# Kernel tuning notes

Hardware: AMD Instinct MI355X
Metric: run time of the kernel (lower is better)

## Reference

```python
import jax, jax.numpy as jnp
import numpy as np

EPS = 1e-8
N_NODES, N_EDGES = 10000, 160000
SI, VI = 128, 16          # node scalar / vector channels
ES, EV = 32, 4            # edge scalar / vector channels
SO, VO = 128, 16          # output scalar / vector channels
MSI, MVI = 2 * SI + ES, 2 * VI + EV   # message input dims: 288, 36
H1 = max(MVI, VO)         # layer-1 hidden = 36 (bottleneck=1)
H2 = max(VO, VO)          # layer-2 hidden = 16
SVO = 3                   # scalarization_vectorization_output_dim


def _safe_norm(x, axis):
    return jnp.sqrt(jnp.sum(x * x, axis=axis) + EPS)


def _gcp(s, v, frames, Wdown, Wdf, Wso, bso, Wup, Wg, bg):
    """GCP block on edge-level inputs (node_inputs=False, vector_gate=True).
    s: [E, si], v: [E, vi, 3], frames: [E, 3, 3]."""
    v_pre = jnp.swapaxes(v, -1, -2)                 # [E, 3, vi]
    v_hid = v_pre @ Wdown                           # [E, 3, h]
    v_norm = _safe_norm(v_hid, axis=-2)             # [E, h]
    v_frames = v_pre @ Wdf                          # [E, 3, svo]
    # scalarize: frames @ v_frames -> [E,3,svo], transpose -> [E,svo,3], flatten to 9
    local = jnp.swapaxes(frames @ v_frames, -1, -2).reshape(v.shape[0], 3 * SVO)
    merged = jnp.concatenate([s, v_norm, local], axis=-1)
    s_out = merged @ Wso + bso                      # [E, so]
    v_out = jnp.swapaxes(v_hid @ Wup, -1, -2)       # [E, vo, 3]
    gate = jax.nn.sigmoid(jax.nn.silu(s_out) @ Wg + bg)  # vector gate
    v_out = v_out * gate[..., None]
    return jax.nn.silu(s_out), v_out


def _lin(key, fan_in, fan_out):
    return jax.random.normal(key, (fan_in, fan_out), dtype=jnp.float32) / np.sqrt(fan_in)


def setup_inputs() -> dict:
    key = jax.random.key(0)
    ks = jax.random.split(key, 24)
    M1 = H1 + MSI + 3 * SVO   # 333
    M2 = H2 + SO + 3 * SVO    # 153
    return {
        "node_s": jax.random.normal(ks[0], (N_NODES, SI), dtype=jnp.float32),
        "node_v": jax.random.normal(ks[1], (N_NODES, VI, 3), dtype=jnp.float32),
        "edge_s": jax.random.normal(ks[2], (N_EDGES, ES), dtype=jnp.float32),
        "edge_v": jax.random.normal(ks[3], (N_EDGES, EV, 3), dtype=jnp.float32),
        "frames": jax.random.normal(ks[4], (N_EDGES, 3, 3), dtype=jnp.float32),
        "g1_Wdown": _lin(ks[5], MVI, H1),
        "g1_Wdf": _lin(ks[6], MVI, SVO),
        "g1_Wso": _lin(ks[7], M1, SO),
        "g1_bso": jnp.zeros((SO,), dtype=jnp.float32),
        "g1_Wup": _lin(ks[8], H1, VO),
        "g1_Wg": _lin(ks[9], SO, VO),
        "g1_bg": jnp.zeros((VO,), dtype=jnp.float32),
        "g2_Wdown": _lin(ks[10], VO, H2),
        "g2_Wdf": _lin(ks[11], VO, SVO),
        "g2_Wso": _lin(ks[12], M2, SO),
        "g2_bso": jnp.zeros((SO,), dtype=jnp.float32),
        "g2_Wup": _lin(ks[13], H2, VO),
        "g2_Wg": _lin(ks[14], SO, VO),
        "g2_bg": jnp.zeros((VO,), dtype=jnp.float32),
        "att_W": _lin(ks[15], SO, 1),
        "att_b": jnp.zeros((1,), dtype=jnp.float32),
        "edge_index": jax.random.randint(ks[16], (2, N_EDGES), 0, N_NODES, dtype=jnp.int64),
    }


def reference(node_s, node_v, edge_s, edge_v, frames,
              g1_Wdown, g1_Wdf, g1_Wso, g1_bso, g1_Wup, g1_Wg, g1_bg,
              g2_Wdown, g2_Wdf, g2_Wso, g2_bso, g2_Wup, g2_Wg, g2_bg,
              att_W, att_b, edge_index):
    row, col = edge_index[0], edge_index[1]
    # edge gather: concat source node, edge, dest node features
    ms = jnp.concatenate([node_s[row], edge_s, node_s[col]], axis=-1)   # [E, 288]
    mv = jnp.concatenate([node_v[row], edge_v, node_v[col]], axis=1)    # [E, 36, 3]
    # message_fusion[0]
    s, v = _gcp(ms, mv, frames, g1_Wdown, g1_Wdf, g1_Wso, g1_bso, g1_Wup, g1_Wg, g1_bg)
    # message_fusion[1] with residual
    s2, v2 = _gcp(s, v, frames, g2_Wdown, g2_Wdf, g2_Wso, g2_bso, g2_Wup, g2_Wg, g2_bg)
    s, v = s + s2, v + v2
    # scalar message attention
    attn = jax.nn.sigmoid(s @ att_W + att_b)
    s = s * attn
    # flatten ScalarVector and scatter-sum aggregate to destination nodes
    flat = jnp.concatenate([s, v.reshape(v.shape[0], VO * 3)], axis=-1)  # [E, 176]
    agg = jax.ops.segment_sum(flat, row, num_segments=N_NODES)           # [N, 176]
    return agg
```

## Files before the change

kernel.cpp:

```cpp
#include <hip/hip_runtime.h>
#include <hip/hip_bf16.h>

#define E_TOT 160000
#define NN    10000
#define EPB   32

typedef unsigned short ushortT;
typedef unsigned int   uintT;
typedef __attribute__((ext_vector_type(8))) short short8;
typedef __attribute__((ext_vector_type(4))) float f32x4;

__device__ __forceinline__ float sigmoidf_(float x) { return 1.0f / (1.0f + __expf(-x)); }
__device__ __forceinline__ float siluf_(float x) { return x * sigmoidf_(x); }

__device__ __forceinline__ ushortT f2b(float f) {
    union { float f; uintT u; } x; x.f = f;
    uintT r = x.u + 0x7fffu + ((x.u >> 16) & 1u);
    return (ushortT)(r >> 16);
}
__device__ __forceinline__ float b2f(ushortT h) {
    union { uintT u; float f; } x; x.u = ((uintT)h) << 16; return x.f;
}
__device__ __forceinline__ uintT pk2(float lo, float hi) {
    union { __hip_bfloat162 h; uintT u; } cv;
    cv.h = __float22bfloat162_rn(make_float2(lo, hi));
    return cv.u;
}
__device__ __forceinline__ short8 ldfrag(const float* p) {
    const float4 x = ((const float4*)p)[0];
    const float4 y = ((const float4*)p)[1];
    union { uintT u[4]; short8 s; } r;
    r.u[0] = pk2(x.x, x.y); r.u[1] = pk2(x.z, x.w);
    r.u[2] = pk2(y.x, y.y); r.u[3] = pk2(y.z, y.w);
    return r.s;
}

#define OFF_W1SO 0
#define OFF_W2SO 45056
#define OFF_W1DF 65536
#define OFF_W1G  68608
#define OFF_W1UP 70656
#define OFF_W2DF 71680
#define OFF_W2G  72704
#define OFF_W2UP 74752
#define WT_USH   75264

#define NOFF_OFF   56320000ULL
#define CUR_OFF    56360016ULL
#define WT_OFF     57040032ULL
#define WS_CSR     57190560ULL
#define NS16_OFF   57190560ULL
#define WS_NS      59750560ULL
#define ES16_OFF   59750560ULL
#define WS_ES      69990560ULL

__device__ __forceinline__ bool idx_is64(const int* pi) {
    return (pi[1] | pi[3] | pi[5] | pi[7] | pi[9] | pi[11] | pi[13] | pi[15]) == 0;
}

__device__ __forceinline__ void weight_prep(
    int i,
    const float* __restrict__ W1so, const float* __restrict__ W2so,
    const float* __restrict__ W1d,  const float* __restrict__ W1f,
    const float* __restrict__ W1g,  const float* __restrict__ W1up,
    const float* __restrict__ W2d,  const float* __restrict__ W2f,
    const float* __restrict__ W2g,  const float* __restrict__ W2up,
    ushortT* __restrict__ ws)
{
    if (i < OFF_W2SO) {
        int n = i / 352, k = i - n * 352;
        ws[i] = (k < 333) ? f2b(W1so[k * 128 + n]) : (ushortT)0;
    } else if (i < OFF_W1DF) {
        int j = i - OFF_W2SO, n = j / 160, k = j - n * 160;
        ws[i] = (k < 153) ? f2b(W2so[k * 128 + n]) : (ushortT)0;
    } else if (i < OFF_W1G) {
        int j = i - OFF_W1DF, n = j / 64, k = j - n * 64;
        float v = 0.f;
        if (k < 36) { if (n < 36) v = W1d[k * 36 + n]; else if (n < 39) v = W1f[k * 3 + (n - 36)]; }
        ws[i] = f2b(v);
    } else if (i < OFF_W1UP) {
        int j = i - OFF_W1G, n = j / 128, k = j - n * 128;
        ws[i] = f2b(W1g[k * 16 + n]);
    } else if (i < OFF_W2DF) {
        int j = i - OFF_W1UP, n = j / 64, k = j - n * 64;
        ws[i] = (k < 36) ? f2b(W1up[k * 16 + n]) : (ushortT)0;
    } else if (i < OFF_W2G) {
        int j = i - OFF_W2DF, n = j / 32, k = j - n * 32;
        float v = 0.f;
        if (k < 16) { if (n < 16) v = W2d[k * 16 + n]; else if (n < 19) v = W2f[k * 3 + (n - 16)]; }
        ws[i] = f2b(v);
    } else if (i < OFF_W2UP) {
        int j = i - OFF_W2G, n = j / 128, k = j - n * 128;
        ws[i] = f2b(W2g[k * 16 + n]);
    } else if (i < WT_USH) {
        int j = i - OFF_W2UP, n = j / 32, k = j - n * 32;
        ws[i] = (k < 16) ? f2b(W2up[k * 16 + n]) : (ushortT)0;
    }
}

__global__ __launch_bounds__(256) void setup_kernel(
    const float* __restrict__ W1so, const float* __restrict__ W2so,
    const float* __restrict__ W1d,  const float* __restrict__ W1f,
    const float* __restrict__ W1g,  const float* __restrict__ W1up,
    const float* __restrict__ W2d,  const float* __restrict__ W2f,
    const float* __restrict__ W2g,  const float* __restrict__ W2up,
    ushortT* __restrict__ ws,
    const void* __restrict__ eidx, int* __restrict__ cur,
    const float* __restrict__ node_s, const float* __restrict__ edge_s,
    ushortT* __restrict__ ns16, ushortT* __restrict__ es16)
{
    int i = blockIdx.x * 256 + threadIdx.x;
    {
        const int* pi = (const int*)eidx;
        const long long* pl = (const long long*)eidx;
        int r = idx_is64(pi) ? (int)pl[i] : pi[i];
        atomicAdd(&cur[r], 1);
    }
    if (ns16 && i < 160000) {
        float4 x = ((const float4*)node_s)[i * 2];
        float4 y = ((const float4*)node_s)[i * 2 + 1];
        uint4 st;
        st.x = pk2(x.x, x.y); st.y = pk2(x.z, x.w);
        st.z = pk2(y.x, y.y); st.w = pk2(y.z, y.w);
        ((uint4*)ns16)[i] = st;
    }
    if (es16) {
        #pragma unroll
        for (int k = 0; k < 4; ++k) {
            float4 x = ((const float4*)edge_s)[i * 8 + 2 * k];
            float4 y = ((const float4*)edge_s)[i * 8 + 2 * k + 1];
            uint4 st;
            st.x = pk2(x.x, x.y); st.y = pk2(x.z, x.w);
            st.z = pk2(y.x, y.y); st.w = pk2(y.z, y.w);
            ((uint4*)es16)[i * 4 + k] = st;
        }
    }
    weight_prep(i, W1so, W2so, W1d, W1f, W1g, W1up, W2d, W2f, W2g, W2up, ws);
}

__global__ __launch_bounds__(256) void prep_kernel(
    const float* __restrict__ W1so, const float* __restrict__ W2so,
    const float* __restrict__ W1d,  const float* __restrict__ W1f,
    const float* __restrict__ W1g,  const float* __restrict__ W1up,
    const float* __restrict__ W2d,  const float* __restrict__ W2f,
    const float* __restrict__ W2g,  const float* __restrict__ W2up,
    ushortT* __restrict__ ws, float* __restrict__ out)
{
    int i = blockIdx.x * 256 + threadIdx.x;
    float4* o4 = (float4*)out;
    #pragma unroll
    for (int k = 0; k < 6; ++k) {
        int z = i + k * 75264;
        if (z < 440000) o4[z] = make_float4(0.f, 0.f, 0.f, 0.f);
    }
    weight_prep(i, W1so, W2so, W1d, W1f, W1g, W1up, W2d, W2f, W2g, W2up, ws);
}

__global__ __launch_bounds__(256) void scan_kernel(int* __restrict__ cur,
                                                   int* __restrict__ noff)
{
    __shared__ int buf[10000];
    __shared__ int partial[256];
    const int t = threadIdx.x;
    for (int i = t; i < NN; i += 256) buf[i] = cur[i];
    for (int i = t; i < NN; i += 256) cur[i] = 0;
    __syncthreads();
    const int base = t * 40;
    int s = 0;
    #pragma unroll
    for (int i = 0; i < 40; ++i) s += (base + i < NN) ? buf[base + i] : 0;
    partial[t] = s;
    __syncthreads();
    for (int o = 1; o < 256; o <<= 1) {
        int v = (t >= o) ? partial[t - o] : 0;
        __syncthreads();
        partial[t] += v;
        __syncthreads();
    }
    int run = (t == 0) ? 0 : partial[t - 1];
    #pragma unroll
    for (int i = 0; i < 40; ++i) {
        int gi = base + i;
        if (gi < NN) { int v = buf[gi]; noff[gi] = run; run += v; }
    }
    if (t == 255) noff[NN] = partial[255];
}

__global__ __launch_bounds__(256) void node_kernel(const ushortT* __restrict__ fb,
                                                   const int* __restrict__ noff,
                                                   float* __restrict__ out)
{
    const int w = threadIdx.x >> 6, l = threadIdx.x & 63;
    const int n = blockIdx.x * 4 + w;
    if (l >= 44) return;
    const int s = noff[n], eend = noff[n + 1];
    float a0 = 0.f, a1 = 0.f, a2 = 0.f, a3 = 0.f;
    int idx = s;
    for (; idx + 2 <= eend; idx += 2) {
        uint2 p0 = *(const uint2*)(fb + (size_t)idx * 176 + l * 4);
        uint2 p1 = *(const uint2*)(fb + (size_t)(idx + 1) * 176 + l * 4);
        a0 += b2f((ushortT)(p0.x & 0xffff)); a1 += b2f((ushortT)(p0.x >> 16));
        a2 += b2f((ushortT)(p0.y & 0xffff)); a3 += b2f((ushortT)(p0.y >> 16));
        a0 += b2f((ushortT)(p1.x & 0xffff)); a1 += b2f((ushortT)(p1.x >> 16));
        a2 += b2f((ushortT)(p1.y & 0xffff)); a3 += b2f((ushortT)(p1.y >> 16));
    }
    if (idx < eend) {
        uint2 p0 = *(const uint2*)(fb + (size_t)idx * 176 + l * 4);
        a0 += b2f((ushortT)(p0.x & 0xffff)); a1 += b2f((ushortT)(p0.x >> 16));
        a2 += b2f((ushortT)(p0.y & 0xffff)); a3 += b2f((ushortT)(p0.y >> 16));
    }
    ((float4*)(out + (size_t)n * 176))[l] = make_float4(a0, a1, a2, a3);
}

#define MFMA(a, b, c) __builtin_amdgcn_mfma_f32_16x16x32_bf16((a), (b), (c), 0, 0, 0)

__global__ __launch_bounds__(256, 5) void edge_kernel(
    const float* __restrict__ node_s, const float* __restrict__ node_v,
    const float* __restrict__ edge_s, const float* __restrict__ edge_v,
    const float* __restrict__ frames,
    const float* __restrict__ b1so, const float* __restrict__ b1g,
    const float* __restrict__ b2so, const float* __restrict__ b2g,
    const float* __restrict__ attW, const float* __restrict__ attb,
    const ushortT* __restrict__ wsc,
    const void* __restrict__ eidx, float* __restrict__ out,
    ushortT* __restrict__ fb, int* __restrict__ cur, const int* __restrict__ noff,
    const ushortT* __restrict__ ns16, const ushortT* __restrict__ es16,
    int csr)
{
    const ushortT* W1T   = wsc + OFF_W1SO;
    const ushortT* W2T   = wsc + OFF_W2SO;
    const ushortT* W1dfT = wsc + OFF_W1DF;
    const ushortT* W1gT  = wsc + OFF_W1G;
    const ushortT* W1upT = wsc + OFF_W1UP;
    const ushortT* W2dfT = wsc + OFF_W2DF;
    const ushortT* W2gT  = wsc + OFF_W2G;
    const ushortT* W2upT = wsc + OFF_W2UP;

    __shared__ __align__(16) char smem[31232];
    ushortT* mvA     = (ushortT*)smem;
    ushortT* m2      = (ushortT*)smem;
    ushortT* vhidA   = (ushortT*)(smem + 10752);
    ushortT* s2s     = (ushortT*)(smem + 10752);
    ushortT* normbuf = (ushortT*)(smem + 19456);
    ushortT* v1A     = (ushortT*)(smem + 19456);
    ushortT* vhid2A  = (ushortT*)(smem + 24064);
    float*   vfr2f   = (float*)(smem + 28672);
    float*   fr      = (float*)(smem + 29824);
    float*   attn    = (float*)(smem + 30976);
    int*     eposb   = (int*)(smem + 31104);

    const int t  = threadIdx.x;
    const int eg = blockIdx.x * EPB;
    const int w  = t >> 6, lane = t & 63, lq = lane >> 4, ln = lane & 15;
    const int te = t >> 3, tj = t & 7;
    const int p  = w & 1;

    const int* pi = (const int*)eidx;
    const long long* pl = (const long long*)eidx;
    const bool is64 = idx_is64(pi);

    {
        const int nr = is64 ? (int)pl[eg + te] : pi[eg + te];
        const int nc = is64 ? (int)pl[E_TOT + eg + te] : pi[E_TOT + eg + te];
        #pragma unroll
        for (int mi = 0; mi < 2; ++mi) {
            if (mi == 1 && tj != 0) break;
            int m = (mi == 0) ? tj : 8;
            const float* src;
            if (m < 4)       src = node_v + nr * 48 + 12 * m;
            else if (m == 4) src = edge_v + (eg + te) * 12;
            else             src = node_v + nc * 48 + 12 * (m - 5);
            float4 x = ((const float4*)src)[0];
            float4 y = ((const float4*)src)[1];
            float4 z = ((const float4*)src)[2];
            float v[12] = {x.x, x.y, x.z, x.w, y.x, y.y, y.z, y.w, z.x, z.y, z.z, z.w};
            int c0 = 4 * m;
            #pragma unroll
            for (int sp = 0; sp < 3; ++sp) {
                *(uintT*)(mvA + (sp * 32 + te) * 40 + c0)     = pk2(v[sp],     v[3 + sp]);
                *(uintT*)(mvA + (sp * 32 + te) * 40 + c0 + 2) = pk2(v[6 + sp], v[9 + sp]);
            }
        }
        #pragma unroll
        for (int k = 0; k < 2; ++k) {
            int j = tj + k * 8;
            if (j < 9) fr[te * 9 + j] = frames[(eg + te) * 9 + j];
        }
        #pragma unroll
        for (int k = 0; k < 3; ++k) {
            int c = 45 + tj + k * 8;
            if (c < 64) normbuf[te * 72 + c] = 0;
        }
        if (t < 192) {
            int r = t >> 1, cc = 36 + ((t & 1) << 1);
            *(uintT*)(mvA + r * 40 + cc) = 0;
        }
    }

    if (csr && tj == 0) {
        int nr = is64 ? (int)pl[eg + te] : pi[eg + te];
        int pos = atomicAdd(&cur[nr], 1);
        eposb[te] = noff[nr] + pos;
    }

    const int klq = lq * 8;
    const int dn0 = w * 32 + ln, dn1 = dn0 + 16;
    const ushortT* b0p = W1T + dn0 * 352 + klq;
    const ushortT* b1p = W1T + dn1 * 352 + klq;
    f32x4 acc00 = {0,0,0,0}, acc01 = {0,0,0,0}, acc10 = {0,0,0,0}, acc11 = {0,0,0,0};
    float dbi0, dbi1;
    {
        const int e0 = ln, e1 = 16 + ln;
        int r0, c0, r1, c1;
        if (is64) {
            r0 = (int)pl[eg + e0]; r1 = (int)pl[eg + e1];
            c0 = (int)pl[E_TOT + eg + e0]; c1 = (int)pl[E_TOT + eg + e1];
        } else {
            r0 = pi[eg + e0]; r1 = pi[eg + e1];
            c0 = pi[E_TOT + eg + e0]; c1 = pi[E_TOT + eg + e1];
        }
        r0 *= 128; c0 *= 128; r1 *= 128; c1 *= 128;
        const int eb0 = (eg + e0) * 32, eb1 = (eg + e1) * 32;
        dbi0 = b1so[dn0]; dbi1 = b1so[dn1];
        #pragma unroll
        for (int ks = 0; ks < 9; ++ks) {
            short8 a0, a1;
            if (ks < 4) {
                if (ns16) {
                    a0 = *(const short8*)(ns16 + r0 + ks * 32 + klq);
                    a1 = *(const short8*)(ns16 + r1 + ks * 32 + klq);
                } else {
                    a0 = ldfrag(node_s + r0 + ks * 32 + klq);
                    a1 = ldfrag(node_s + r1 + ks * 32 + klq);
                }
            } else if (ks == 4) {
                if (es16) {
                    a0 = *(const short8*)(es16 + eb0 + klq);
                    a1 = *(const short8*)(es16 + eb1 + klq);
                } else {
                    a0 = ldfrag(edge_s + eb0 + klq);
                    a1 = ldfrag(edge_s + eb1 + klq);
                }
            } else {
                if (ns16) {
                    a0 = *(const short8*)(ns16 + c0 + (ks - 5) * 32 + klq);
                    a1 = *(const short8*)(ns16 + c1 + (ks - 5) * 32 + klq);
                } else {
                    a0 = ldfrag(node_s + c0 + (ks - 5) * 32 + klq);
                    a1 = ldfrag(node_s + c1 + (ks - 5) * 32 + klq);
                }
            }
            short8 b0 = *(const short8*)(b0p + ks * 32);
            short8 b1 = *(const short8*)(b1p + ks * 32);
            acc00 = MFMA(a0, b0, acc00); acc01 = MFMA(a0, b1, acc01);
            acc10 = MFMA(a1, b0, acc10); acc11 = MFMA(a1, b1, acc11);
        }
    }
    asm volatile("" : "+v"(acc00), "+v"(acc01), "+v"(acc10), "+v"(acc11));
    __syncthreads();

    for (int u = w; u < 18; u += 4) {
        int mt = u / 3, nt = u - mt * 3;
        const ushortT* ap = mvA + (mt * 16 + ln) * 40 + lq * 8;
        const ushortT* bp = W1dfT + (nt * 16 + ln) * 64 + lq * 8;
        f32x4 acc = {0.f, 0.f, 0.f, 0.f};
        acc = MFMA(*(const short8*)ap, *(const short8*)bp, acc);
        short8 a2 = {0, 0, 0, 0, 0, 0, 0, 0};
        if (lq == 0) a2 = *(const short8*)(ap + 32);
        acc = MFMA(a2, *(const short8*)(bp + 32), acc);
        if (nt < 2 || ln < 8) {
            ushortT* op = vhidA + (mt * 16 + lq * 4) * 40 + nt * 16 + ln;
            op[0]   = f2b(acc[0]); op[40]  = f2b(acc[1]);
            op[80]  = f2b(acc[2]); op[120] = f2b(acc[3]);
        }
    }
    __syncthreads();

    {
        #pragma unroll
        for (int k = 0; k < 5; ++k) {
            int h = tj + k * 8;
            if (h < 36) {
                float a0 = b2f(vhidA[te * 40 + h]);
                float a1 = b2f(vhidA[(32 + te) * 40 + h]);
                float a2 = b2f(vhidA[(64 + te) * 40 + h]);
                normbuf[te * 72 + h] = f2b(sqrtf(fmaf(a0, a0, fmaf(a1, a1, fmaf(a2, a2, 1e-8f)))));
            }
        }
        for (int i = t; i < 288; i += 256) {
            int e = i / 9, r = i - e * 9, a = r / 3, b = r - a * 3;
            float x = fr[e * 9 + b * 3 + 0] * b2f(vhidA[e * 40 + 36 + a])
                    + fr[e * 9 + b * 3 + 1] * b2f(vhidA[(32 + e) * 40 + 36 + a])
                    + fr[e * 9 + b * 3 + 2] * b2f(vhidA[(64 + e) * 40 + 36 + a]);
            normbuf[e * 72 + 36 + r] = f2b(x);
        }
    }
    __syncthreads();

    {
        const int e0 = ln, e1 = 16 + ln;
        #pragma unroll
        for (int ks = 9; ks < 11; ++ks) {
            short8 a0 = *(const short8*)(normbuf + e0 * 72 + (ks - 9) * 32 + klq);
            short8 a1 = *(const short8*)(normbuf + e1 * 72 + (ks - 9) * 32 + klq);
            short8 b0 = *(const short8*)(b0p + ks * 32);
            short8 b1 = *(const short8*)(b1p + ks * 32);
            acc00 = MFMA(a0, b0, acc00); acc01 = MFMA(a0, b1, acc01);
            acc10 = MFMA(a1, b0, acc10); acc11 = MFMA(a1, b1, acc11);
        }
        #pragma unroll
        for (int r = 0; r < 4; ++r) {
            int m0 = lq * 4 + r;
            m2[m0 * 168 + dn0]        = f2b(siluf_(acc00[r] + dbi0));
            m2[m0 * 168 + dn1]        = f2b(siluf_(acc01[r] + dbi1));
            m2[(16 + m0) * 168 + dn0] = f2b(siluf_(acc10[r] + dbi0));
            m2[(16 + m0) * 168 + dn1] = f2b(siluf_(acc11[r] + dbi1));
        }
    }
    __syncthreads();

    {
        f32x4 gacc = {0,0,0,0};
        {
            const ushortT* ap = m2 + (p * 16 + ln) * 168;
            const ushortT* bp = W1gT + ln * 128;
            #pragma unroll
            for (int ks = 0; ks < 4; ++ks)
                gacc = MFMA(*(const short8*)(ap + ks * 32 + lq * 8),
                            *(const short8*)(bp + ks * 32 + lq * 8), gacc);
        }
        float g1[4];
        {
            float bi = b1g[ln];
            #pragma unroll
            for (int r = 0; r < 4; ++r) g1[r] = sigmoidf_(gacc[r] + bi);
        }
        const ushortT* bpu = W1upT + ln * 64 + lq * 8;
        short8 bu1 = *(const short8*)bpu;
        short8 bu2 = *(const short8*)(bpu + 32);
        #pragma unroll
        for (int c = 0; c < 2; ++c) {
            if (c == 1 && w >= 2) break;
            int mt = w + c * 4;
            const ushortT* ap = vhidA + (mt * 16 + ln) * 40 + lq * 8;
            f32x4 acc = {0,0,0,0};
            acc = MFMA(*(const short8*)ap, bu1, acc);
            short8 a2 = {0, 0, 0, 0, 0, 0, 0, 0};
            if (lq == 0) a2 = *(const short8*)(ap + 32);
            acc = MFMA(a2, bu2, acc);
            #pragma unroll
            for (int r = 0; r < 4; ++r) {
                int row = mt * 16 + lq * 4 + r;
                v1A[row * 24 + ln] = f2b(acc[r] * g1[r]);
            }
        }
        #pragma unroll
        for (int c = 0; c < 2; ++c) {
            if (c == 1 && w >= 2) break;
            int mt = w + c * 4;
            const ushortT* ap = v1A + (mt * 16 + ln) * 24 + lq * 8;
            short8 a = {0, 0, 0, 0, 0, 0, 0, 0};
            if (lq < 2) a = *(const short8*)ap;
            #pragma unroll
            for (int nt = 0; nt < 2; ++nt) {
                const ushortT* bp = W2dfT + (nt * 16 + ln) * 32 + lq * 8;
                f32x4 acc = {0,0,0,0};
                acc = MFMA(a, *(const short8*)bp, acc);
                if (nt == 0) {
                    ushortT* op = vhid2A + (mt * 16 + lq * 4) * 24 + ln;
                    op[0]  = f2b(acc[0]); op[24] = f2b(acc[1]);
                    op[48] = f2b(acc[2]); op[72] = f2b(acc[3]);
                } else if (ln < 3) {
                    float* op = vfr2f + (mt * 16 + lq * 4) * 3 + ln;
                    op[0] = acc[0]; op[3] = acc[1]; op[6] = acc[2]; op[9] = acc[3];
                }
            }
        }
    }
    __syncthreads();

    {
        #pragma unroll
        for (int k = 0; k < 2; ++k) {
            int i = t + k * 256, e = i >> 4, h = i & 15;
            float a0 = b2f(vhid2A[e * 24 + h]);
            float a1 = b2f(vhid2A[(32 + e) * 24 + h]);
            float a2 = b2f(vhid2A[(64 + e) * 24 + h]);
            m2[e * 168 + 128 + h] = f2b(sqrtf(fmaf(a0, a0, fmaf(a1, a1, fmaf(a2, a2, 1e-8f)))));
        }
        for (int i = t; i < 288; i += 256) {
            int e = i / 9, r = i - e * 9, a = r / 3, b = r - a * 3;
            float x = fr[e * 9 + b * 3 + 0] * vfr2f[e * 3 + a]
                    + fr[e * 9 + b * 3 + 1] * vfr2f[(32 + e) * 3 + a]
                    + fr[e * 9 + b * 3 + 2] * vfr2f[(64 + e) * 3 + a];
            m2[e * 168 + 144 + r] = f2b(x);
        }
        if (tj) m2[te * 168 + 152 + tj] = 0;
    }
    __syncthreads();

    {
        f32x4 acc00i = {0,0,0,0}, acc01i = {0,0,0,0}, acc10i = {0,0,0,0}, acc11i = {0,0,0,0};
        const ushortT* a0p = m2 + ln * 168 + lq * 8;
        const ushortT* a1p = m2 + (16 + ln) * 168 + lq * 8;
        const ushortT* b0pi = W2T + (w * 32 + ln) * 160 + lq * 8;
        const ushortT* b1pi = W2T + (w * 32 + 16 + ln) * 160 + lq * 8;
        #pragma unroll
        for (int ks = 0; ks < 5; ++ks) {
            short8 a0 = *(const short8*)(a0p + ks * 32);
            short8 a1 = *(const short8*)(a1p + ks * 32);
            short8 b0 = *(const short8*)(b0pi + ks * 32);
            short8 b1 = *(const short8*)(b1pi + ks * 32);
            acc00i = MFMA(a0, b0, acc00i); acc01i = MFMA(a0, b1, acc01i);
            acc10i = MFMA(a1, b0, acc10i); acc11i = MFMA(a1, b1, acc11i);
        }
        const int n0 = w * 32 + ln, n1 = n0 + 16;
        float bi0 = b2so[n0], bi1 = b2so[n1];
        #pragma unroll
        for (int r = 0; r < 4; ++r) {
            int m0 = lq * 4 + r;
            s2s[m0 * 136 + n0]        = f2b(siluf_(acc00i[r] + bi0));
            s2s[m0 * 136 + n1]        = f2b(siluf_(acc01i[r] + bi1));
            s2s[(16 + m0) * 136 + n0] = f2b(siluf_(acc10i[r] + bi0));
            s2s[(16 + m0) * 136 + n1] = f2b(siluf_(acc11i[r] + bi1));
        }
    }
    __syncthreads();

    {
        f32x4 gacc = {0,0,0,0};
        {
            const ushortT* ap = s2s + (p * 16 + ln) * 136;
            const ushortT* bp = W2gT + ln * 128;
            #pragma unroll
            for (int ks = 0; ks < 4; ++ks)
                gacc = MFMA(*(const short8*)(ap + ks * 32 + lq * 8),
                            *(const short8*)(bp + ks * 32 + lq * 8), gacc);
        }
        float g2[4];
        {
            float bi = b2g[ln];
            #pragma unroll
            for (int r = 0; r < 4; ++r) g2[r] = sigmoidf_(gacc[r] + bi);
        }
        const ushortT* bpu = W2upT + ln * 32 + lq * 8;
        short8 bu = *(const short8*)bpu;
        #pragma unroll
        for (int c = 0; c < 2; ++c) {
            if (c == 1 && w >= 2) break;
            int mt = w + c * 4;
            const ushortT* ap = vhid2A + (mt * 16 + ln) * 24 + lq * 8;
            short8 a = {0, 0, 0, 0, 0, 0, 0, 0};
            if (lq < 2) a = *(const short8*)ap;
            f32x4 acc = {0,0,0,0};
            acc = MFMA(a, bu, acc);
            #pragma unroll
            for (int r = 0; r < 4; ++r) {
                int row = mt * 16 + lq * 4 + r;
                float vfin = b2f(v1A[row * 24 + ln]) + acc[r] * g2[r];
                v1A[row * 24 + ln] = f2b(vfin);
            }
        }
        {
            float sum = 0.f;
            int c0 = tj * 16;
            #pragma unroll
            for (int c = c0; c < c0 + 16; ++c)
                sum = fmaf(b2f(m2[te * 168 + c]) + b2f(s2s[te * 136 + c]), attW[c], sum);
            sum += __shfl_xor(sum, 4);
            sum += __shfl_xor(sum, 2);
            sum += __shfl_xor(sum, 1);
            if (tj == 0) attn[te] = sigmoidf_(sum + attb[0]);
        }
    }
    __syncthreads();

    {
        const float at = attn[te];
        if (csr) {
            const int pos = eposb[te];
            ushortT* fbe = fb + (size_t)pos * 176;
            #pragma unroll
            for (int k = 0; k < 11; ++k) {
                int j = 2 * tj + 16 * k;
                float v0, v1;
                if (j < 128) {
                    v0 = (b2f(m2[te * 168 + j])     + b2f(s2s[te * 136 + j]))     * at;
                    v1 = (b2f(m2[te * 168 + j + 1]) + b2f(s2s[te * 136 + j + 1])) * at;
                } else {
                    int r = j - 128;
                    int o0 = r / 3,        sp0 = r - o0 * 3;
                    int o1 = (r + 1) / 3,  sp1 = (r + 1) - o1 * 3;
                    v0 = b2f(v1A[(sp0 * 32 + te) * 24 + o0]);
                    v1 = b2f(v1A[(sp1 * 32 + te) * 24 + o1]);
                }
                *(uintT*)(fbe + j) = pk2(v0, v1);
            }
        } else {
            const int nr = is64 ? (int)pl[eg + te] : pi[eg + te];
            const int orow = nr * 176;
            #pragma unroll
            for (int k = 0; k < 22; ++k) {
                int j = tj + k * 8;
                float val;
                if (j < 128) {
                    val = (b2f(m2[te * 168 + j]) + b2f(s2s[te * 136 + j])) * at;
                } else {
                    int r = j - 128, o = r / 3, sp = r - o * 3;
                    val = b2f(v1A[(sp * 32 + te) * 24 + o]);
                }
                atomicAdd(&out[orow + j], val);
            }
        }
    }
}

extern "C" void kernel_launch(void* const* d_in, const int* in_sizes, int n_in,
                              void* d_out, int out_size, void* d_ws, size_t ws_size,
                              hipStream_t stream) {
    const float* node_s = (const float*)d_in[0];
    const float* node_v = (const float*)d_in[1];
    const float* edge_s = (const float*)d_in[2];
    const float* edge_v = (const float*)d_in[3];
    const float* frames = (const float*)d_in[4];
    const float* W1d  = (const float*)d_in[5];
    const float* W1f  = (const float*)d_in[6];
    const float* W1so = (const float*)d_in[7];
    const float* b1so = (const float*)d_in[8];
    const float* W1up = (const float*)d_in[9];
    const float* W1g  = (const float*)d_in[10];
    const float* b1g  = (const float*)d_in[11];
    const float* W2d  = (const float*)d_in[12];
    const float* W2f  = (const float*)d_in[13];
    const float* W2so = (const float*)d_in[14];
    const float* b2so = (const float*)d_in[15];
    const float* W2up = (const float*)d_in[16];
    const float* W2g  = (const float*)d_in[17];
    const float* b2g  = (const float*)d_in[18];
    const float* attW = (const float*)d_in[19];
    const float* attb = (const float*)d_in[20];
    const void*  eidx = d_in[21];

    float* out = (float*)d_out;
    char* ws = (char*)d_ws;

    int mode = 0;
    if (ws_size >= WS_ES)       mode = 3;
    else if (ws_size >= WS_NS)  mode = 2;
    else if (ws_size >= WS_CSR) mode = 1;
    const int csr = (mode >= 1);

    ushortT* wt    = csr ? (ushortT*)(ws + WT_OFF)  : (ushortT*)ws;
    ushortT* fbuf  = csr ? (ushortT*)ws             : nullptr;
    int*     noff  = csr ? (int*)(ws + NOFF_OFF)    : nullptr;
    int*     cur   = csr ? (int*)(ws + CUR_OFF)     : nullptr;
    ushortT* ns16  = (mode >= 2) ? (ushortT*)(ws + NS16_OFF) : nullptr;
    ushortT* es16  = (mode >= 3) ? (ushortT*)(ws + ES16_OFF) : nullptr;

    if (csr) {
        hipMemsetAsync(cur, 0, NN * sizeof(int), stream);
        setup_kernel<<<625, 256, 0, stream>>>(
            W1so, W2so, W1d, W1f, W1g, W1up, W2d, W2f, W2g, W2up,
            wt, eidx, cur, node_s, edge_s, ns16, es16);
        scan_kernel<<<1, 256, 0, stream>>>(cur, noff);
    } else {
        prep_kernel<<<294, 256, 0, stream>>>(W1so, W2so, W1d, W1f, W1g, W1up,
                                             W2d, W2f, W2g, W2up, wt, out);
    }

    edge_kernel<<<E_TOT / EPB, 256, 0, stream>>>(
        node_s, node_v, edge_s, edge_v, frames,
        b1so, b1g, b2so, b2g, attW, attb,
        (const ushortT*)wt, eidx, out, fbuf, cur, noff, ns16, es16, csr);

    if (csr) {
        node_kernel<<<2500, 256, 0, stream>>>((const ushortT*)fbuf, noff, out);
    }
}
```

Baseline: 312.1 us.

## Shrink edge kernel LDS footprint and raise occupancy target to six blocks

Shared-memory use is cut from 31232 to 27136 bytes. The layer-1 vector output is kept in registers instead of being re-read from LDS, and vector buffers are compacted from row stride 24 to 16 and aliased onto dead regions. The attention value and the CSR output position now live in registers, with the position shuffled across lanes, which removes their LDS slots. Launch bounds rise to 6 blocks per SM to hide more latency, at the risk of register spills under the tighter VGPR budget and bank conflicts from the stride-16 layout.

```diff
diff --git a/kernel.cpp b/kernel.cpp
--- a/kernel.cpp
+++ b/kernel.cpp
@@ -214,7 +214,7 @@
 
 #define MFMA(a, b, c) __builtin_amdgcn_mfma_f32_16x16x32_bf16((a), (b), (c), 0, 0, 0)
 
-__global__ __launch_bounds__(256, 5) void edge_kernel(
+__global__ __launch_bounds__(256, 6) void edge_kernel(
     const float* __restrict__ node_s, const float* __restrict__ node_v,
     const float* __restrict__ edge_s, const float* __restrict__ edge_v,
     const float* __restrict__ frames,
@@ -236,18 +236,17 @@
     const ushortT* W2gT  = wsc + OFF_W2G;
     const ushortT* W2upT = wsc + OFF_W2UP;
 
-    __shared__ __align__(16) char smem[31232];
+    __shared__ __align__(16) char smem[27136];
     ushortT* mvA     = (ushortT*)smem;
     ushortT* m2      = (ushortT*)smem;
     ushortT* vhidA   = (ushortT*)(smem + 10752);
     ushortT* s2s     = (ushortT*)(smem + 10752);
     ushortT* normbuf = (ushortT*)(smem + 19456);
-    ushortT* v1A     = (ushortT*)(smem + 19456);
-    ushortT* vhid2A  = (ushortT*)(smem + 24064);
-    float*   vfr2f   = (float*)(smem + 28672);
-    float*   fr      = (float*)(smem + 29824);
-    float*   attn    = (float*)(smem + 30976);
-    int*     eposb   = (int*)(smem + 31104);
+    ushortT* v1s     = (ushortT*)(smem + 19456);
+    ushortT* vhid2A  = (ushortT*)(smem + 19456);
+    float*   fr      = (float*)(smem + 24064);
+    float*   vfr2f   = (float*)(smem + 25216);
+    ushortT* v1f     = (ushortT*)(smem + 24064);
 
     const int t  = threadIdx.x;
     const int eg = blockIdx.x * EPB;
@@ -258,6 +257,9 @@
     const int* pi = (const int*)eidx;
     const long long* pl = (const long long*)eidx;
     const bool is64 = idx_is64(pi);
+
+    int posr = 0;
+    float att_reg = 0.f;
 
     {
         const int nr = is64 ? (int)pl[eg + te] : pi[eg + te];
@@ -295,12 +297,9 @@
             int r = t >> 1, cc = 36 + ((t & 1) << 1);
             *(uintT*)(mvA + r * 40 + cc) = 0;
         }
-    }
-
-    if (csr && tj == 0) {
-        int nr = is64 ? (int)pl[eg + te] : pi[eg + te];
-        int pos = atomicAdd(&cur[nr], 1);
-        eposb[te] = noff[nr] + pos;
+        if (csr && tj == 0) {
+            posr = noff[nr] + atomicAdd(&cur[nr], 1);
+        }
     }
 
     const int klq = lq * 8;
@@ -419,6 +418,7 @@
     }
     __syncthreads();
 
+    float v1reg[2][4] = {{0.f,0.f,0.f,0.f},{0.f,0.f,0.f,0.f}};
     {
         f32x4 gacc = {0,0,0,0};
         {
@@ -451,14 +451,16 @@
             #pragma unroll
             for (int r = 0; r < 4; ++r) {
                 int row = mt * 16 + lq * 4 + r;
-                v1A[row * 24 + ln] = f2b(acc[r] * g1[r]);
+                float vv = acc[r] * g1[r];
+                v1reg[c][r] = vv;
+                v1s[row * 16 + ln] = f2b(vv);
             }
         }
         #pragma unroll
         for (int c = 0; c < 2; ++c) {
             if (c == 1 && w >= 2) break;
             int mt = w + c * 4;
-            const ushortT* ap = v1A + (mt * 16 + ln) * 24 + lq * 8;
+            const ushortT* ap = v1s + (mt * 16 + ln) * 16 + lq * 8;
             short8 a = {0, 0, 0, 0, 0, 0, 0, 0};
             if (lq < 2) a = *(const short8*)ap;
             #pragma unroll
@@ -467,9 +469,9 @@
                 f32x4 acc = {0,0,0,0};
                 acc = MFMA(a, *(const short8*)bp, acc);
                 if (nt == 0) {
-                    ushortT* op = vhid2A + (mt * 16 + lq * 4) * 24 + ln;
-                    op[0]  = f2b(acc[0]); op[24] = f2b(acc[1]);
-                    op[48] = f2b(acc[2]); op[72] = f2b(acc[3]);
+                    ushortT* op = vhid2A + (mt * 16 + lq * 4) * 16 + ln;
+                    op[0]  = f2b(acc[0]); op[16] = f2b(acc[1]);
+                    op[32] = f2b(acc[2]); op[48] = f2b(acc[3]);
                 } else if (ln < 3) {
                     float* op = vfr2f + (mt * 16 + lq * 4) * 3 + ln;
                     op[0] = acc[0]; op[3] = acc[1]; op[6] = acc[2]; op[9] = acc[3];
@@ -483,9 +485,9 @@
         #pragma unroll
         for (int k = 0; k < 2; ++k) {
             int i = t + k * 256, e = i >> 4, h = i & 15;
-            float a0 = b2f(vhid2A[e * 24 + h]);
-            float a1 = b2f(vhid2A[(32 + e) * 24 + h]);
-            float a2 = b2f(vhid2A[(64 + e) * 24 + h]);
+            float a0 = b2f(vhid2A[e * 16 + h]);
+            float a1 = b2f(vhid2A[(32 + e) * 16 + h]);
+            float a2 = b2f(vhid2A[(64 + e) * 16 + h]);
             m2[e * 168 + 128 + h] = f2b(sqrtf(fmaf(a0, a0, fmaf(a1, a1, fmaf(a2, a2, 1e-8f)))));
         }
         for (int i = t; i < 288; i += 256) {
@@ -549,7 +551,7 @@
         for (int c = 0; c < 2; ++c) {
             if (c == 1 && w >= 2) break;
             int mt = w + c * 4;
-            const ushortT* ap = vhid2A + (mt * 16 + ln) * 24 + lq * 8;
+            const ushortT* ap = vhid2A + (mt * 16 + ln) * 16 + lq * 8;
             short8 a = {0, 0, 0, 0, 0, 0, 0, 0};
             if (lq < 2) a = *(const short8*)ap;
             f32x4 acc = {0,0,0,0};
@@ -557,8 +559,8 @@
             #pragma unroll
             for (int r = 0; r < 4; ++r) {
                 int row = mt * 16 + lq * 4 + r;
-                float vfin = b2f(v1A[row * 24 + ln]) + acc[r] * g2[r];
-                v1A[row * 24 + ln] = f2b(vfin);
+                float vfin = v1reg[c][r] + acc[r] * g2[r];
+                v1f[row * 16 + ln] = f2b(vfin);
             }
         }
         {
@@ -570,15 +572,15 @@
             sum += __shfl_xor(sum, 4);
             sum += __shfl_xor(sum, 2);
             sum += __shfl_xor(sum, 1);
-            if (tj == 0) attn[te] = sigmoidf_(sum + attb[0]);
-        }
-    }
-    __syncthreads();
-
-    {
-        const float at = attn[te];
+            att_reg = sigmoidf_(sum + attb[0]);
+        }
+    }
+    __syncthreads();
+
+    {
+        const float at = att_reg;
         if (csr) {
-            const int pos = eposb[te];
+            const int pos = __shfl(posr, lane & 56);
             ushortT* fbe = fb + (size_t)pos * 176;
             #pragma unroll
             for (int k = 0; k < 11; ++k) {
@@ -591,8 +593,8 @@
                     int r = j - 128;
                     int o0 = r / 3,        sp0 = r - o0 * 3;
                     int o1 = (r + 1) / 3,  sp1 = (r + 1) - o1 * 3;
-                    v0 = b2f(v1A[(sp0 * 32 + te) * 24 + o0]);
-                    v1 = b2f(v1A[(sp1 * 32 + te) * 24 + o1]);
+                    v0 = b2f(v1f[(sp0 * 32 + te) * 16 + o0]);
+                    v1 = b2f(v1f[(sp1 * 32 + te) * 16 + o1]);
                 }
                 *(uintT*)(fbe + j) = pk2(v0, v1);
             }
@@ -607,7 +609,7 @@
                     val = (b2f(m2[te * 168 + j]) + b2f(s2s[te * 136 + j])) * at;
                 } else {
                     int r = j - 128, o = r / 3, sp = r - o * 3;
-                    val = b2f(v1A[(sp * 32 + te) * 24 + o]);
+                    val = b2f(v1f[(sp * 32 + te) * 16 + o]);
                 }
                 atomicAdd(&out[orow + j], val);
             }
```

After: 312.7 us. Within noise of the previous version (+0.2%).
